# Optimization experiments

Measured on AMD Instinct MI355X. Metric: run time of the kernel, lower is better.

The kernel has to match this reference:

```python
import jax, jax.numpy as jnp
import numpy as np


def setup_inputs() -> dict:
    key = jax.random.key(0)
    k0, k1, k2, k3 = jax.random.split(key, 4)
    B, N, D, C, F = 8192, 784, 64, 10, 2  # batch, input_dim, bond_dim, num_classes, feature_dim
    x = jax.random.uniform(k0, (B, N), dtype=jnp.float32)  # pixel values in [0,1]
    core0 = jax.random.normal(k1, (F, 1, D), dtype=jnp.float32) * 0.1
    base = jnp.broadcast_to(jnp.eye(D, dtype=jnp.float32), (N - 2, F, D, D))
    cores_mid = base + jax.random.normal(k2, (N - 2, F, D, D), dtype=jnp.float32) * 0.01
    core_last = jax.random.normal(k3, (F, D, C), dtype=jnp.float32) * 0.1
    return {"x": x, "core0": core0, "cores_mid": cores_mid, "core_last": core_last}


def reference(x, core0, cores_mid, core_last):
    EPS = 1e-8
    factor = jnp.float32(np.pi / 2.0)
    # FeatureMap: [B, N] -> [B, N, 2] with (cos, sin)
    feats = jnp.stack([jnp.cos(factor * x), jnp.sin(factor * x)], axis=-1)
    # First site: M = v0 @ A0.squeeze(1)  -> [B, D]
    M = jnp.einsum('bf,fd->bd', feats[:, 0, :], core0[:, 0, :])
    # Sequential left->right contraction over middle sites with per-step L2 normalization
    v_mid = jnp.moveaxis(feats[:, 1:-1, :], 1, 0)  # [N-2, B, 2]

    def step(M, inp):
        v, A = inp  # v: [B, 2], A: [2, D, D]
        Mn = jnp.einsum('bi,bf,fij->bj', M, v, A)
        Mn = Mn / (jnp.linalg.norm(Mn, axis=1, keepdims=True) + EPS)
        return Mn, None

    M, _ = jax.lax.scan(step, M, (v_mid, cores_mid))
    # Last site: logits[b,c] = sum_i M[b,i] * (v_N[b,f] A_N[f,i,c])
    logits = jnp.einsum('bi,bf,fic->bc', M, feats[:, -1, :], core_last)
    return logits
```

## Files before the change

kernel.cpp:

```cpp
#include <hip/hip_runtime.h>

typedef __attribute__((ext_vector_type(8))) short s16x8;
typedef __attribute__((ext_vector_type(4))) float f32x4;
typedef __attribute__((ext_vector_type(4))) int i32x4;

#define NMID 782
#define PI_2 1.5707963267948966f
#define EG_STEP_BYTES 16384
#define EG_ELEMS ((size_t)NMID * 8192)
#define SLAB_B 2304

__device__ __forceinline__ int cvt_pk_bf16(float a, float b) {
  int r;
  asm("v_cvt_pk_bf16_f32 %0, %1, %2" : "=v"(r) : "v"(a), "v"(b));
  return r;
}

__device__ __forceinline__ f32x4 mfma_bf16(i32x4 a, i32x4 b, f32x4 c) {
  return __builtin_amdgcn_mfma_f32_16x16x32_bf16(
      __builtin_bit_cast(s16x8, a), __builtin_bit_cast(s16x8, b), c, 0, 0, 0);
}

__device__ __forceinline__ unsigned short bf16_rne(float v) {
  unsigned u = __float_as_uint(v);
  return (unsigned short)((u + 0x7FFFu + ((u >> 16) & 1)) >> 16);
}

__global__ __launch_bounds__(256) void prep_eg(const float* __restrict__ cm,
                                               unsigned short* __restrict__ eg) {
  const int n = blockIdx.x;
  const float* src = cm + (size_t)n * 8192;
  unsigned short* dst = eg + (size_t)n * 8192;
#pragma unroll
  for (int it = 0; it < 4; ++it) {
    int row = it * 256 + threadIdx.x;
    int q = row >> 6, l = row & 63;
    int t = q >> 2, cc = q & 3;
    int f = cc >> 1, c2 = cc & 1, h = l >> 4;
    int j = 16 * t + (l & 15);
    unsigned short v8[8];
#pragma unroll
    for (int e = 0; e < 8; ++e) {
      int i = 32 * c2 + 16 * (e >> 2) + 4 * h + (e & 3);
      float val = src[(f * 64 + i) * 64 + j] - (i == j ? 1.0f : 0.0f);
      v8[e] = bf16_rne(val);
    }
    *(uint4*)(dst + (size_t)row * 8) = *(const uint4*)v8;
  }
}

#define STEP4(nc, CUR, NXT, CC, SS)                                         \
  {                                                                         \
    int np = (nc) + 3;                                                      \
    if (np >= NMID) np = NMID - 1;                                          \
    const char* pnxt = base + (size_t)np * EG_STEP_BYTES;                   \
    _Pragma("unroll") for (int q = 0; q < 4; ++q)                           \
        NXT[q] = *(const i32x4*)(pnxt + q * 1024);                          \
    float cps = (CC) + (SS);                                                \
    f32x4 z = {0.f, 0.f, 0.f, 0.f};                                         \
    f32x4 accA = mfma_bf16(CUR[0], B0, z);                                  \
    accA = mfma_bf16(CUR[1], B1, accA);                                     \
    f32x4 accB = mfma_bf16(CUR[2], B0, z);                                  \
    accB = mfma_bf16(CUR[3], B1, accB);                                     \
    f32x4 mn;                                                               \
    _Pragma("unroll") for (int r = 0; r < 4; ++r)                           \
        mn[r] = cps * own4[r] + (CC)*accA[r] + (SS)*accB[r];                \
    own4 = mn;                                                              \
    int2 wq;                                                                \
    wq.x = cvt_pk_bf16(mn[0], mn[1]);                                       \
    wq.y = cvt_pk_bf16(mn[2], mn[3]);                                       \
    *(int2*)(xlds + (((nc) + 1) & 1) * SLAB_B + bl * 144 + h * 32 +         \
             wv * 8) = wq;                                                  \
    asm volatile("s_waitcnt lgkmcnt(0)" ::: "memory");                      \
    __builtin_amdgcn_s_barrier();                                           \
    __builtin_amdgcn_sched_barrier(0);                                      \
    {                                                                       \
      const char* rb =                                                      \
          xlds + (((nc) + 1) & 1) * SLAB_B + bl * 144 + h * 32;             \
      B0 = *(const i32x4*)(rb);                                             \
      B1 = *(const i32x4*)(rb + 16);                                        \
    }                                                                       \
  }

__global__ __launch_bounds__(256) void mps_main(
    const float* __restrict__ x, const float* __restrict__ core0,
    const float* __restrict__ core_last, const unsigned short* __restrict__ eg,
    float* __restrict__ out) {
  __shared__ alignas(16) char xlds[2 * SLAB_B];
  const int lane = threadIdx.x & 63;
  const int wv = threadIdx.x >> 6;
  const int bl = lane & 15;
  const int h = lane >> 4;
  const int b = blockIdx.x * 16 + bl;
  const float* xr = x + (size_t)b * 784;
  const char* base = (const char*)eg + (size_t)wv * 4096 + (size_t)lane * 16;

  f32x4 own4;
  i32x4 B0, B1;
  {
    float xv = xr[0];
    float s, c;
    __sincosf(PI_2 * xv, &s, &c);
    float fm[16];
#pragma unroll
    for (int t = 0; t < 4; ++t)
#pragma unroll
      for (int r = 0; r < 4; ++r) {
        int j = 16 * t + 4 * h + r;
        fm[t * 4 + r] = c * core0[j] + s * core0[64 + j];
      }
#pragma unroll
    for (int r = 0; r < 4; ++r) own4[r] = fm[wv * 4 + r];
#pragma unroll
    for (int p = 0; p < 4; ++p) {
      B0[p] = cvt_pk_bf16(fm[2 * p], fm[2 * p + 1]);
      B1[p] = cvt_pk_bf16(fm[8 + 2 * p], fm[8 + 2 * p + 1]);
    }
  }

  i32x4 frA[4], frB[4], frC[4], frD[4];
#pragma unroll
  for (int q = 0; q < 4; ++q)
    frA[q] = *(const i32x4*)(base + 0 * EG_STEP_BYTES + q * 1024);
#pragma unroll
  for (int q = 0; q < 4; ++q)
    frB[q] = *(const i32x4*)(base + 1 * EG_STEP_BYTES + q * 1024);
#pragma unroll
  for (int q = 0; q < 4; ++q)
    frC[q] = *(const i32x4*)(base + 2 * EG_STEP_BYTES + q * 1024);

  float xq[12], xqn[12];
  *(f32x4*)&xq[0] = *(const f32x4*)(xr + 0);
  *(f32x4*)&xq[4] = *(const f32x4*)(xr + 4);
  *(f32x4*)&xq[8] = *(const f32x4*)(xr + 8);

  for (int g = 0; g < 97; ++g) {
    if (g < 96) {
      const float* xp = xr + 8 * (g + 1);
      *(f32x4*)&xqn[0] = *(const f32x4*)(xp + 0);
      *(f32x4*)&xqn[4] = *(const f32x4*)(xp + 4);
      *(f32x4*)&xqn[8] = *(const f32x4*)(xp + 8);
    } else {
      *(f32x4*)&xqn[0] = *(const f32x4*)(xr + 776);
      *(f32x4*)&xqn[4] = *(const f32x4*)(xr + 780);
    }

    float cg[8], sg[8];
#pragma unroll
    for (int k = 0; k < 8; ++k) __sincosf(PI_2 * xq[1 + k], &sg[k], &cg[k]);

    if ((g & 7) == 0) {
      float ss = 0.f;
#pragma unroll
      for (int p = 0; p < 4; ++p) {
        unsigned u0 = (unsigned)B0[p], u1 = (unsigned)B1[p];
        float a0 = __uint_as_float(u0 << 16);
        float a1 = __uint_as_float(u0 & 0xFFFF0000u);
        float b0f = __uint_as_float(u1 << 16);
        float b1f = __uint_as_float(u1 & 0xFFFF0000u);
        ss += a0 * a0 + a1 * a1 + b0f * b0f + b1f * b1f;
      }
      ss += __shfl_xor(ss, 16);
      ss += __shfl_xor(ss, 32);
      float inv = rsqrtf(ss);
      cg[0] *= inv;
      sg[0] *= inv;
    }

    int n0 = 8 * g;
    STEP4(n0 + 0, frA, frD, cg[0], sg[0]);
    STEP4(n0 + 1, frB, frA, cg[1], sg[1]);
    STEP4(n0 + 2, frC, frB, cg[2], sg[2]);
    STEP4(n0 + 3, frD, frC, cg[3], sg[3]);
    STEP4(n0 + 4, frA, frD, cg[4], sg[4]);
    STEP4(n0 + 5, frB, frA, cg[5], sg[5]);
    STEP4(n0 + 6, frC, frB, cg[6], sg[6]);
    STEP4(n0 + 7, frD, frC, cg[7], sg[7]);

#pragma unroll
    for (int i = 0; i < 12; ++i) xq[i] = xqn[i];
  }

  {
    float cg[6], sg[6];
#pragma unroll
    for (int k = 0; k < 6; ++k) __sincosf(PI_2 * xq[1 + k], &sg[k], &cg[k]);
    STEP4(776, frA, frD, cg[0], sg[0]);
    STEP4(777, frB, frA, cg[1], sg[1]);
    STEP4(778, frC, frB, cg[2], sg[2]);
    STEP4(779, frD, frC, cg[3], sg[3]);
    STEP4(780, frA, frD, cg[4], sg[4]);
    STEP4(781, frB, frA, cg[5], sg[5]);
  }

  asm volatile("s_waitcnt lgkmcnt(0)" ::: "memory");
  __builtin_amdgcn_s_barrier();
  *(f32x4*)(xlds + wv * 1152 + lane * 16) = own4;
  asm volatile("s_waitcnt lgkmcnt(0)" ::: "memory");
  __builtin_amdgcn_s_barrier();
  __builtin_amdgcn_sched_barrier(0);
  float fm[16];
#pragma unroll
  for (int t = 0; t < 4; ++t) {
    f32x4 v = *(const f32x4*)(xlds + t * 1152 + lane * 16);
#pragma unroll
    for (int r = 0; r < 4; ++r) fm[t * 4 + r] = v[r];
  }

  float ss = 0.f;
#pragma unroll
  for (int i = 0; i < 16; ++i) ss += fm[i] * fm[i];
  ss += __shfl_xor(ss, 16);
  ss += __shfl_xor(ss, 32);
  float inv = 1.0f / (sqrtf(ss) + 1e-8f);
#pragma unroll
  for (int i = 0; i < 16; ++i) fm[i] *= inv;

  float xv = xq[7];
  float s, c;
  __sincosf(PI_2 * xv, &s, &c);
  float part[10];
#pragma unroll
  for (int cc = 0; cc < 10; ++cc) part[cc] = 0.f;
#pragma unroll
  for (int t = 0; t < 4; ++t)
#pragma unroll
    for (int r = 0; r < 4; ++r) {
      int i = 16 * t + 4 * h + r;
      float mv = fm[t * 4 + r];
#pragma unroll
      for (int cc = 0; cc < 10; ++cc)
        part[cc] += mv * (c * core_last[i * 10 + cc] + s * core_last[640 + i * 10 + cc]);
    }
#pragma unroll
  for (int cc = 0; cc < 10; ++cc) {
    part[cc] += __shfl_xor(part[cc], 16);
    part[cc] += __shfl_xor(part[cc], 32);
  }
  if (wv == 0 && h == 0) {
#pragma unroll
    for (int cc = 0; cc < 10; ++cc) out[b * 10 + cc] = part[cc];
  }
}

__global__ __launch_bounds__(64) void mps_slow(const float* __restrict__ x,
                                               const float* __restrict__ core0,
                                               const float* __restrict__ cm,
                                               const float* __restrict__ cl,
                                               float* __restrict__ out) {
  int b = blockIdx.x * 64 + threadIdx.x;
  float m[64], mn[64];
  float s, c;
  __sincosf(PI_2 * x[(size_t)b * 784], &s, &c);
  for (int d = 0; d < 64; ++d) m[d] = c * core0[d] + s * core0[64 + d];
  for (int n = 0; n < NMID; ++n) {
    __sincosf(PI_2 * x[(size_t)b * 784 + n + 1], &s, &c);
    const float* A0 = cm + (size_t)n * 8192;
    const float* A1 = A0 + 4096;
    for (int j = 0; j < 64; ++j) mn[j] = 0.f;
    for (int i = 0; i < 64; ++i) {
      float w0 = c * m[i], w1 = s * m[i];
      for (int j = 0; j < 64; ++j) mn[j] += w0 * A0[i * 64 + j] + w1 * A1[i * 64 + j];
    }
    float ssn = 0.f;
    for (int j = 0; j < 64; ++j) ssn += mn[j] * mn[j];
    float inv = 1.f / (sqrtf(ssn) + 1e-8f);
    for (int j = 0; j < 64; ++j) m[j] = mn[j] * inv;
  }
  __sincosf(PI_2 * x[(size_t)b * 784 + 783], &s, &c);
  for (int cc = 0; cc < 10; ++cc) {
    float acc = 0.f;
    for (int i = 0; i < 64; ++i)
      acc += m[i] * (c * cl[i * 10 + cc] + s * cl[640 + i * 10 + cc]);
    out[b * 10 + cc] = acc;
  }
}

extern "C" void kernel_launch(void* const* d_in, const int* in_sizes, int n_in,
                              void* d_out, int out_size, void* d_ws, size_t ws_size,
                              hipStream_t stream) {
  const float* x = (const float*)d_in[0];
  const float* core0 = (const float*)d_in[1];
  const float* cm = (const float*)d_in[2];
  const float* cl = (const float*)d_in[3];
  float* out = (float*)d_out;
  size_t need = EG_ELEMS * sizeof(unsigned short);
  if (ws_size >= need) {
    unsigned short* eg = (unsigned short*)d_ws;
    prep_eg<<<NMID, 256, 0, stream>>>(cm, eg);
    mps_main<<<512, 256, 0, stream>>>(x, core0, cl, eg, out);
  } else {
    mps_slow<<<8192 / 64, 64, 0, stream>>>(x, core0, cm, cl, out);
  }
}
```

Baseline: 267.9 us.

## Interleave per-step sincos, raise MFMA priority, relayout LDS exchange, request two blocks per CU

Each step now computes its own sincos inside the step macro, so the trig work sits next to the MFMAs instead of being batched up front. The MFMA section is wrapped in s_setprio so it is favoured over other waves. The LDS exchange buffer is relaid out with a new stride pattern, likely to cut bank conflicts. The x prefetch is restructured to use rolling registers, and launch bounds ask for two blocks per CU. Together these aim to hide latency and raise occupancy, at the cost of register pressure limits and more LDS use.

```diff
diff --git a/kernel.cpp b/kernel.cpp
--- a/kernel.cpp
+++ b/kernel.cpp
@@ -8,7 +8,7 @@
 #define PI_2 1.5707963267948966f
 #define EG_STEP_BYTES 16384
 #define EG_ELEMS ((size_t)NMID * 8192)
-#define SLAB_B 2304
+#define XCH_PAR 3072
 
 __device__ __forceinline__ int cvt_pk_bf16(float a, float b) {
   int r;
@@ -49,44 +49,50 @@
   }
 }
 
-#define STEP4(nc, CUR, NXT, CC, SS)                                         \
+#define STEP1G(nc, CUR, NXT, Xv, RS)                                        \
   {                                                                         \
     int np = (nc) + 3;                                                      \
     if (np >= NMID) np = NMID - 1;                                          \
     const char* pnxt = base + (size_t)np * EG_STEP_BYTES;                   \
     _Pragma("unroll") for (int q = 0; q < 4; ++q)                           \
         NXT[q] = *(const i32x4*)(pnxt + q * 1024);                          \
-    float cps = (CC) + (SS);                                                \
+    float c0, s0;                                                           \
+    __sincosf(PI_2 * (Xv), &s0, &c0);                                       \
+    c0 *= (RS);                                                             \
+    s0 *= (RS);                                                             \
     f32x4 z = {0.f, 0.f, 0.f, 0.f};                                         \
-    f32x4 accA = mfma_bf16(CUR[0], B0, z);                                  \
-    accA = mfma_bf16(CUR[1], B1, accA);                                     \
-    f32x4 accB = mfma_bf16(CUR[2], B0, z);                                  \
-    accB = mfma_bf16(CUR[3], B1, accB);                                     \
+    __builtin_amdgcn_s_setprio(1);                                          \
+    f32x4 aA = mfma_bf16(CUR[0], B0, z);                                    \
+    aA = mfma_bf16(CUR[1], B1, aA);                                         \
+    f32x4 aB = mfma_bf16(CUR[2], B0, z);                                    \
+    aB = mfma_bf16(CUR[3], B1, aB);                                         \
+    __builtin_amdgcn_s_setprio(0);                                          \
+    float cps = c0 + s0;                                                    \
     f32x4 mn;                                                               \
     _Pragma("unroll") for (int r = 0; r < 4; ++r)                           \
-        mn[r] = cps * own4[r] + (CC)*accA[r] + (SS)*accB[r];                \
+        mn[r] = cps * own4[r] + c0 * aA[r] + s0 * aB[r];                    \
     own4 = mn;                                                              \
     int2 wq;                                                                \
     wq.x = cvt_pk_bf16(mn[0], mn[1]);                                       \
     wq.y = cvt_pk_bf16(mn[2], mn[3]);                                       \
-    *(int2*)(xlds + (((nc) + 1) & 1) * SLAB_B + bl * 144 + h * 32 +         \
+    *(int2*)(xlds + (((nc) + 1) & 1) * XCH_PAR + h * 768 + bl * 48 +        \
              wv * 8) = wq;                                                  \
     asm volatile("s_waitcnt lgkmcnt(0)" ::: "memory");                      \
     __builtin_amdgcn_s_barrier();                                           \
     __builtin_amdgcn_sched_barrier(0);                                      \
     {                                                                       \
       const char* rb =                                                      \
-          xlds + (((nc) + 1) & 1) * SLAB_B + bl * 144 + h * 32;             \
+          xlds + (((nc) + 1) & 1) * XCH_PAR + h * 768 + bl * 48;            \
       B0 = *(const i32x4*)(rb);                                             \
       B1 = *(const i32x4*)(rb + 16);                                        \
     }                                                                       \
   }
 
-__global__ __launch_bounds__(256) void mps_main(
+__global__ __launch_bounds__(256, 2) void mps_main(
     const float* __restrict__ x, const float* __restrict__ core0,
     const float* __restrict__ core_last, const unsigned short* __restrict__ eg,
     float* __restrict__ out) {
-  __shared__ alignas(16) char xlds[2 * SLAB_B];
+  __shared__ alignas(16) char xlds[2 * XCH_PAR];
   const int lane = threadIdx.x & 63;
   const int wv = threadIdx.x >> 6;
   const int bl = lane & 15;
@@ -98,9 +104,8 @@
   f32x4 own4;
   i32x4 B0, B1;
   {
-    float xv = xr[0];
     float s, c;
-    __sincosf(PI_2 * xv, &s, &c);
+    __sincosf(PI_2 * xr[0], &s, &c);
     float fm[16];
 #pragma unroll
     for (int t = 0; t < 4; ++t)
@@ -129,26 +134,27 @@
   for (int q = 0; q < 4; ++q)
     frC[q] = *(const i32x4*)(base + 2 * EG_STEP_BYTES + q * 1024);
 
-  float xq[12], xqn[12];
+  float xq[12];
+  f32x4 xfA, xfB;
   *(f32x4*)&xq[0] = *(const f32x4*)(xr + 0);
   *(f32x4*)&xq[4] = *(const f32x4*)(xr + 4);
   *(f32x4*)&xq[8] = *(const f32x4*)(xr + 8);
 
   for (int g = 0; g < 97; ++g) {
-    if (g < 96) {
-      const float* xp = xr + 8 * (g + 1);
-      *(f32x4*)&xqn[0] = *(const f32x4*)(xp + 0);
-      *(f32x4*)&xqn[4] = *(const f32x4*)(xp + 4);
-      *(f32x4*)&xqn[8] = *(const f32x4*)(xp + 8);
-    } else {
-      *(f32x4*)&xqn[0] = *(const f32x4*)(xr + 776);
-      *(f32x4*)&xqn[4] = *(const f32x4*)(xr + 780);
-    }
-
-    float cg[8], sg[8];
-#pragma unroll
-    for (int k = 0; k < 8; ++k) __sincosf(PI_2 * xq[1 + k], &sg[k], &cg[k]);
-
+    if (g > 0) {
+#pragma unroll
+      for (int i = 0; i < 4; ++i) xq[i] = xq[8 + i];
+      *(f32x4*)&xq[4] = xfA;
+      *(f32x4*)&xq[8] = xfB;
+    }
+    {
+      int xo = (g < 96) ? 8 * g + 12 : 780;
+      int xo2 = (g < 96) ? 8 * g + 16 : 780;
+      xfA = *(const f32x4*)(xr + xo);
+      xfB = *(const f32x4*)(xr + xo2);
+    }
+
+    float rs = 1.0f;
     if ((g & 7) == 0) {
       float ss = 0.f;
 #pragma unroll
@@ -156,41 +162,36 @@
         unsigned u0 = (unsigned)B0[p], u1 = (unsigned)B1[p];
         float a0 = __uint_as_float(u0 << 16);
         float a1 = __uint_as_float(u0 & 0xFFFF0000u);
-        float b0f = __uint_as_float(u1 << 16);
-        float b1f = __uint_as_float(u1 & 0xFFFF0000u);
-        ss += a0 * a0 + a1 * a1 + b0f * b0f + b1f * b1f;
+        float d0 = __uint_as_float(u1 << 16);
+        float d1 = __uint_as_float(u1 & 0xFFFF0000u);
+        ss += a0 * a0 + a1 * a1 + d0 * d0 + d1 * d1;
       }
       ss += __shfl_xor(ss, 16);
       ss += __shfl_xor(ss, 32);
-      float inv = rsqrtf(ss);
-      cg[0] *= inv;
-      sg[0] *= inv;
+      rs = rsqrtf(ss);
     }
 
     int n0 = 8 * g;
-    STEP4(n0 + 0, frA, frD, cg[0], sg[0]);
-    STEP4(n0 + 1, frB, frA, cg[1], sg[1]);
-    STEP4(n0 + 2, frC, frB, cg[2], sg[2]);
-    STEP4(n0 + 3, frD, frC, cg[3], sg[3]);
-    STEP4(n0 + 4, frA, frD, cg[4], sg[4]);
-    STEP4(n0 + 5, frB, frA, cg[5], sg[5]);
-    STEP4(n0 + 6, frC, frB, cg[6], sg[6]);
-    STEP4(n0 + 7, frD, frC, cg[7], sg[7]);
-
-#pragma unroll
-    for (int i = 0; i < 12; ++i) xq[i] = xqn[i];
+    STEP1G(n0 + 0, frA, frD, xq[1], rs);
+    STEP1G(n0 + 1, frB, frA, xq[2], 1.0f);
+    STEP1G(n0 + 2, frC, frB, xq[3], 1.0f);
+    STEP1G(n0 + 3, frD, frC, xq[4], 1.0f);
+    STEP1G(n0 + 4, frA, frD, xq[5], 1.0f);
+    STEP1G(n0 + 5, frB, frA, xq[6], 1.0f);
+    STEP1G(n0 + 6, frC, frB, xq[7], 1.0f);
+    STEP1G(n0 + 7, frD, frC, xq[8], 1.0f);
   }
 
   {
-    float cg[6], sg[6];
-#pragma unroll
-    for (int k = 0; k < 6; ++k) __sincosf(PI_2 * xq[1 + k], &sg[k], &cg[k]);
-    STEP4(776, frA, frD, cg[0], sg[0]);
-    STEP4(777, frB, frA, cg[1], sg[1]);
-    STEP4(778, frC, frB, cg[2], sg[2]);
-    STEP4(779, frD, frC, cg[3], sg[3]);
-    STEP4(780, frA, frD, cg[4], sg[4]);
-    STEP4(781, frB, frA, cg[5], sg[5]);
+#pragma unroll
+    for (int i = 0; i < 4; ++i) xq[i] = xq[8 + i];
+    *(f32x4*)&xq[4] = xfA;
+    STEP1G(776, frA, frD, xq[1], 1.0f);
+    STEP1G(777, frB, frA, xq[2], 1.0f);
+    STEP1G(778, frC, frB, xq[3], 1.0f);
+    STEP1G(779, frD, frC, xq[4], 1.0f);
+    STEP1G(780, frA, frD, xq[5], 1.0f);
+    STEP1G(781, frB, frA, xq[6], 1.0f);
   }
 
   asm volatile("s_waitcnt lgkmcnt(0)" ::: "memory");
```

Result: faster. 251.1 us (-6.3%).
